# Optimization experiments

Measured on AMD Instinct MI355X. Metric: run time of the kernel, lower is better.

## Reference

```python
import jax, jax.numpy as jnp
import numpy as np

B, C, H, W = 4, 128, 64, 64


def setup_inputs() -> dict:
    key = jax.random.key(0)
    k1, k2 = jax.random.split(key)
    x = jax.random.normal(k1, (B, C, H, W), dtype=jnp.float32)
    # 1x1 conv kv_mapper: weight [C_out, C_in], bias [C_out]; C_out == C_in == C
    W_kv = jax.random.normal(k2, (C, C), dtype=jnp.float32) * (1.0 / np.sqrt(C))
    b_kv = jnp.zeros((C,), dtype=jnp.float32)
    return {"x": x, "W_kv": W_kv, "b_kv": b_kv}


def reference(x, W_kv, b_kv):
    b, c, h, w = x.shape
    # kv_mapper: 1x1 conv  -> v: [b, c, h, w]
    v = jnp.einsum('bchw,oc->bohw', x, W_kv) + b_kv[None, :, None, None]
    # rearrange 'b c h w -> b (h w) c'
    L = h * w
    values = v.reshape(b, c, L).transpose(0, 2, 1)    # keys == values
    queries = x.reshape(b, c, L).transpose(0, 2, 1)
    # scaled dot-product attention, full [b, L, L] scores
    scores = jnp.einsum('blc,btc->blt', queries, values) / jnp.sqrt(jnp.asarray(c, x.dtype))
    attn = jax.nn.softmax(scores, axis=-1)
    out = jnp.einsum('blt,btv->blv', attn, values)    # [b, L, c]
    # rearrange 'b (h w) c -> b c h w'
    return out.transpose(0, 2, 1).reshape(b, c, h, w)
```

## Files before the change

### kernel.cpp

```cpp
#include <hip/hip_runtime.h>

#define LQ 4096
#define CH 128
#define NB 4
#define QSCALE 0.12753139626233174f
#define MAXCH 8
#define TILE_HW 8192

#if defined(__has_builtin)
#if __has_builtin(__builtin_amdgcn_mfma_f32_16x16x16bf16_1k)
#define HAVE_MFMA16 1
#endif
#endif

typedef __attribute__((ext_vector_type(8))) unsigned short ushort8;
typedef __attribute__((ext_vector_type(4))) unsigned short ushort4v;
typedef __attribute__((ext_vector_type(4))) short short4v;
typedef __attribute__((ext_vector_type(8))) __bf16 bf16x8;
typedef __attribute__((ext_vector_type(4))) float f32x4;

__device__ inline unsigned short f2bf(float f) {
    unsigned int u = __builtin_bit_cast(unsigned int, f);
    u += 0x7fffu + ((u >> 16) & 1u);
    return (unsigned short)(u >> 16);
}
__device__ inline float bf2f(unsigned short h) {
    unsigned int u = (unsigned int)h << 16;
    return __builtin_bit_cast(float, u);
}
__device__ inline unsigned int bfpack2(float a, float b) {
    unsigned int ua = __builtin_bit_cast(unsigned int, a) + 0x8000u;
    unsigned int ub = __builtin_bit_cast(unsigned int, b) + 0x8000u;
    return (ua >> 16) | (ub & 0xffff0000u);
}
__device__ inline void gload_lds16(const unsigned short* g, unsigned short* l) {
    __builtin_amdgcn_global_load_lds(
        (const __attribute__((address_space(1))) unsigned int*)(g),
        (__attribute__((address_space(3))) unsigned int*)(l), 16, 0, 0);
}

__global__ __launch_bounds__(256) void prep_kernel(
    const float* __restrict__ x, const float* __restrict__ Wkv,
    const float* __restrict__ bkv,
    unsigned short* __restrict__ Vt2, unsigned short* __restrict__ Vc2)
{
    __shared__ __align__(16) unsigned short xs[64 * 136];
    __shared__ __align__(16) unsigned short vs[128 * 72];
    const int tid = threadIdx.x;
    const int lane = tid & 63;
    const int wave = tid >> 6;
    const int quad = lane >> 4, l16 = lane & 15;
    const int b = blockIdx.x & 3;
    const int T = blockIdx.x >> 2;
    const int l0 = T << 6;

    {
        const f32x4* xg4 = (const f32x4*)(x + (size_t)b * CH * LQ + l0);
        #pragma unroll
        for (int i = 0; i < 8; ++i) {
            int idx = i * 256 + tid;
            int c = idx >> 4, l4 = idx & 15;
            f32x4 v = xg4[c * (LQ / 4) + l4];
            #pragma unroll
            for (int m = 0; m < 4; ++m) xs[(l4 * 4 + m) * 136 + c] = f2bf(v[m]);
        }
    }
    __syncthreads();

    const int wo = wave * 32;
    f32x4 acc[2][4];
    #pragma unroll
    for (int ot = 0; ot < 2; ++ot)
        #pragma unroll
        for (int lt = 0; lt < 4; ++lt) acc[ot][lt] = f32x4{0.f, 0.f, 0.f, 0.f};

    #pragma unroll
    for (int kc = 0; kc < 4; ++kc) {
        bf16x8 af[2];
        #pragma unroll
        for (int ot = 0; ot < 2; ++ot) {
            const float* wrow = Wkv + (size_t)(wo + ot * 16 + l16) * CH + kc * 32 + quad * 8;
            ushort8 a;
            #pragma unroll
            for (int j = 0; j < 8; ++j) a[j] = f2bf(wrow[j]);
            af[ot] = __builtin_bit_cast(bf16x8, a);
        }
        #pragma unroll
        for (int lt = 0; lt < 4; ++lt) {
            bf16x8 bf = __builtin_bit_cast(bf16x8,
                *(const ushort8*)(xs + (lt * 16 + l16) * 136 + kc * 32 + quad * 8));
            #pragma unroll
            for (int ot = 0; ot < 2; ++ot)
                acc[ot][lt] = __builtin_amdgcn_mfma_f32_16x16x32_bf16(af[ot], bf, acc[ot][lt], 0, 0, 0);
        }
    }
    #pragma unroll
    for (int ot = 0; ot < 2; ++ot) {
        float bias[4];
        #pragma unroll
        for (int r = 0; r < 4; ++r) bias[r] = bkv[wo + ot * 16 + quad * 4 + r];
        #pragma unroll
        for (int lt = 0; lt < 4; ++lt)
            #pragma unroll
            for (int r = 0; r < 4; ++r)
                vs[(wo + ot * 16 + quad * 4 + r) * 72 + lt * 16 + l16] =
                    f2bf(acc[ot][lt][r] + bias[r]);
    }
    __syncthreads();
    const size_t tbase = ((size_t)b * 64 + T) * TILE_HW;
    #pragma unroll
    for (int i = 0; i < 4; ++i) {
        const int ci = i * 256 + tid;
        const int g = ci >> 6, ls = ci & 63;
        const int nt = g >> 2, kc = g & 3, qs = ls >> 4, l16s = ls & 15;
        ushort8 v;
        #pragma unroll
        for (int j = 0; j < 8; ++j) v[j] = vs[(kc * 32 + qs * 8 + j) * 72 + nt * 16 + l16s];
        *(ushort8*)(Vt2 + tbase + (size_t)ci * 8) = v;
    }
    #pragma unroll
    for (int i = 0; i < 4; ++i) {
        const int ci = i * 256 + tid;
        const int g = ci >> 6, ls = ci & 63;
        const int nt = g >> 2, p = g & 3, qs = ls >> 4, l16s = ls & 15;
        ushort4v a = *(const ushort4v*)(vs + (p * 32 + l16s) * 72 + nt * 16 + qs * 4);
        ushort4v c2 = *(const ushort4v*)(vs + (p * 32 + 16 + l16s) * 72 + nt * 16 + qs * 4);
        ushort8 v;
        #pragma unroll
        for (int j = 0; j < 4; ++j) { v[j] = a[j]; v[j + 4] = c2[j]; }
        *(ushort8*)(Vc2 + tbase + (size_t)ci * 8) = v;
    }
}

__global__ __launch_bounds__(256) void attn_kernel(
    const float* __restrict__ x, const unsigned short* __restrict__ Vt2,
    const unsigned short* __restrict__ Vc2,
    unsigned short* __restrict__ Opart, float* __restrict__ Lsum, int titers)
{
    __shared__ __align__(16) unsigned short bufA[2][TILE_HW];
    __shared__ __align__(16) unsigned short bufB[2][TILE_HW];
    const int tid = threadIdx.x;
    const int wave = tid >> 6, lane = tid & 63;
    const int quad = lane >> 4, l16 = lane & 15;
    const int b = blockIdx.x & 3;
    const int rest = blockIdx.x >> 2;
    const int qtile = rest & 31;
    const int chunk = rest >> 5;
    const int q0w = (qtile << 7) + (wave << 5);
    const int Tbase = chunk * titers;

    const unsigned short* vtb = Vt2 + (size_t)b * 64 * TILE_HW;
    const unsigned short* vcb = Vc2 + (size_t)b * 64 * TILE_HW;

    bf16x8 qf[2][4];
    #pragma unroll
    for (int mt = 0; mt < 2; ++mt)
        #pragma unroll
        for (int kc = 0; kc < 4; ++kc) {
            ushort8 v;
            #pragma unroll
            for (int j = 0; j < 8; ++j) {
                int c = kc * 32 + quad * 8 + j;
                v[j] = f2bf(x[((size_t)b * CH + c) * LQ + q0w + mt * 16 + l16] * QSCALE);
            }
            qf[mt][kc] = __builtin_bit_cast(bf16x8, v);
        }

    f32x4 oacc[2][8];
    #pragma unroll
    for (int mt = 0; mt < 2; ++mt)
        #pragma unroll
        for (int i = 0; i < 8; ++i) oacc[mt][i] = f32x4{0.f, 0.f, 0.f, 0.f};
    float lsum[2] = {0.f, 0.f};

    auto issue = [&](int T, int nb) {
        const unsigned short* sa = vtb + (size_t)T * TILE_HW + lane * 8;
        const unsigned short* sb = vcb + (size_t)T * TILE_HW + lane * 8;
        #pragma unroll
        for (int g = 0; g < 4; ++g) {
            const int go = (wave * 4 + g) * 512;
            gload_lds16(sa + go, &bufA[nb][go]);
            gload_lds16(sb + go, &bufB[nb][go]);
        }
    };
    issue(Tbase, 0);

    for (int it = 0; it < titers; ++it) {
        __syncthreads();
        if (it + 1 < titers) issue(Tbase + it + 1, (it + 1) & 1);
        const unsigned short* A = bufA[it & 1];
        const unsigned short* B = bufB[it & 1];

        f32x4 s[2][4];
        #pragma unroll
        for (int nt = 0; nt < 4; ++nt) {
            bf16x8 vA[4];
            #pragma unroll
            for (int kc = 0; kc < 4; ++kc)
                vA[kc] = __builtin_bit_cast(bf16x8,
                    *(const ushort8*)(A + (nt * 4 + kc) * 512 + lane * 8));
            #pragma unroll
            for (int mt = 0; mt < 2; ++mt) {
                s[mt][nt] = f32x4{0.f, 0.f, 0.f, 0.f};
                #pragma unroll
                for (int kc = 0; kc < 4; ++kc)
                    s[mt][nt] = __builtin_amdgcn_mfma_f32_16x16x32_bf16(
                        vA[kc], qf[mt][kc], s[mt][nt], 0, 0, 0);
            }
        }
#ifdef HAVE_MFMA16
        short4v pf[2][4];
#else
        bf16x8 pf[2][4];
#endif
        #pragma unroll
        for (int nt = 0; nt < 4; ++nt)
            #pragma unroll
            for (int mt = 0; mt < 2; ++mt) {
                float p0 = __builtin_amdgcn_exp2f(s[mt][nt][0]);
                float p1 = __builtin_amdgcn_exp2f(s[mt][nt][1]);
                float p2 = __builtin_amdgcn_exp2f(s[mt][nt][2]);
                float p3 = __builtin_amdgcn_exp2f(s[mt][nt][3]);
                lsum[mt] += (p0 + p1) + (p2 + p3);
                unsigned int lo = bfpack2(p0, p1);
                unsigned int hi = bfpack2(p2, p3);
#ifdef HAVE_MFMA16
                ushort4v pk;
                pk[0] = (unsigned short)lo; pk[1] = (unsigned short)(lo >> 16);
                pk[2] = (unsigned short)hi; pk[3] = (unsigned short)(hi >> 16);
                pf[mt][nt] = __builtin_bit_cast(short4v, pk);
#else
                ushort8 pk;
                pk[0] = (unsigned short)lo; pk[1] = (unsigned short)(lo >> 16);
                pk[2] = (unsigned short)hi; pk[3] = (unsigned short)(hi >> 16);
                pk[4] = 0; pk[5] = 0; pk[6] = 0; pk[7] = 0;
                pf[mt][nt] = __builtin_bit_cast(bf16x8, pk);
#endif
            }
        #pragma unroll
        for (int nt = 0; nt < 4; ++nt) {
            #pragma unroll
            for (int p = 0; p < 4; ++p) {
                ushort8 d8 = *(const ushort8*)(B + (nt * 4 + p) * 512 + lane * 8);
                #pragma unroll
                for (int h = 0; h < 2; ++h) {
                    ushort4v f;
                    #pragma unroll
                    for (int j = 0; j < 4; ++j) f[j] = d8[h * 4 + j];
#ifdef HAVE_MFMA16
                    short4v vB = __builtin_bit_cast(short4v, f);
                    #pragma unroll
                    for (int mt = 0; mt < 2; ++mt)
                        oacc[mt][p * 2 + h] = __builtin_amdgcn_mfma_f32_16x16x16bf16_1k(
                            pf[mt][nt], vB, oacc[mt][p * 2 + h], 0, 0, 0);
#else
                    ushort8 vb;
                    #pragma unroll
                    for (int j = 0; j < 4; ++j) { vb[j] = f[j]; vb[j + 4] = 0; }
                    bf16x8 vB = __builtin_bit_cast(bf16x8, vb);
                    #pragma unroll
                    for (int mt = 0; mt < 2; ++mt)
                        oacc[mt][p * 2 + h] = __builtin_amdgcn_mfma_f32_16x16x32_bf16(
                            pf[mt][nt], vB, oacc[mt][p * 2 + h], 0, 0, 0);
#endif
                }
            }
        }
    }
    const size_t pbase = ((size_t)(chunk * NB + b) * LQ);
    #pragma unroll
    for (int mt = 0; mt < 2; ++mt) {
        float v = lsum[mt];
        v += __shfl_xor(v, 16);
        v += __shfl_xor(v, 32);
        if (lane < 16) Lsum[pbase + q0w + mt * 16 + lane] = v;
    }
    #pragma unroll
    for (int mt = 0; mt < 2; ++mt)
        #pragma unroll
        for (int r = 0; r < 4; ++r) {
            const int q = q0w + mt * 16 + quad * 4 + r;
            unsigned short* orow = Opart + (pbase + q) * CH + l16;
            #pragma unroll
            for (int nc = 0; nc < 8; ++nc) orow[nc * 16] = f2bf(oacc[mt][nc][r]);
        }
}

__global__ __launch_bounds__(256) void combine_kernel(
    const unsigned short* __restrict__ Opart, const float* __restrict__ Lsum,
    float* __restrict__ out, int nchunk)
{
    __shared__ __align__(16) float ls[32 * 132];
    __shared__ float linv[32];
    const int tid = threadIdx.x;
    const int b = blockIdx.x & 3;
    const int q0 = (blockIdx.x >> 2) << 5;

    if (tid < 32) {
        float s = 0.f;
        for (int ch = 0; ch < nchunk; ++ch) s += Lsum[(size_t)(ch * NB + b) * LQ + q0 + tid];
        linv[tid] = 1.0f / s;
    }
    __syncthreads();
    {
        const int c8 = (tid & 15) * 8, qg = tid >> 4;
        #pragma unroll
        for (int i = 0; i < 2; ++i) {
            const int q = qg * 2 + i;
            float s[8];
            #pragma unroll
            for (int k = 0; k < 8; ++k) s[k] = 0.f;
            for (int ch = 0; ch < nchunk; ++ch) {
                ushort8 p = *(const ushort8*)(Opart +
                    ((size_t)(ch * NB + b) * LQ + q0 + q) * CH + c8);
                #pragma unroll
                for (int k = 0; k < 8; ++k) s[k] += bf2f(p[k]);
            }
            const float li = linv[q];
            f32x4 o0, o1;
            #pragma unroll
            for (int k = 0; k < 4; ++k) { o0[k] = s[k] * li; o1[k] = s[k + 4] * li; }
            *(f32x4*)(ls + q * 132 + c8) = o0;
            *(f32x4*)(ls + q * 132 + c8 + 4) = o1;
        }
    }
    __syncthreads();
    {
        const int c = tid & 127, qh = tid >> 7;
        float* dst = out + ((size_t)b * CH + c) * LQ + q0 + qh * 16;
        #pragma unroll
        for (int i = 0; i < 4; ++i) {
            f32x4 o;
            #pragma unroll
            for (int r = 0; r < 4; ++r) o[r] = ls[(qh * 16 + i * 4 + r) * 132 + c];
            ((f32x4*)dst)[i] = o;
        }
    }
}

extern "C" void kernel_launch(void* const* d_in, const int* in_sizes, int n_in,
                              void* d_out, int out_size, void* d_ws, size_t ws_size,
                              hipStream_t stream) {
    const float* x   = (const float*)d_in[0];
    const float* Wkv = (const float*)d_in[1];
    const float* bkv = (const float*)d_in[2];
    float* out = (float*)d_out;

    const size_t vElems = (size_t)NB * LQ * CH;
    unsigned short* Vt2 = (unsigned short*)d_ws;
    unsigned short* Vc2 = Vt2 + vElems;
    float* Lsum = (float*)(Vc2 + vElems);
    unsigned short* Opart = (unsigned short*)(Lsum + (size_t)MAXCH * NB * LQ);

    int nchunk = 4;
    const size_t fixed = 2 * vElems * 2 + (size_t)MAXCH * NB * LQ * 4;
    while (nchunk > 1 && fixed + (size_t)nchunk * NB * LQ * CH * 2 > ws_size) nchunk >>= 1;
    const int titers = (LQ / 64) / nchunk;

    prep_kernel<<<dim3(256), dim3(256), 0, stream>>>(x, Wkv, bkv, Vt2, Vc2);
    attn_kernel<<<dim3(128 * nchunk), dim3(256), 0, stream>>>(x, Vt2, Vc2, Opart, Lsum, titers);
    combine_kernel<<<dim3(512), dim3(256), 0, stream>>>(Opart, Lsum, out, nchunk);
}
```

Before: 122.1 us.

## Single-buffer A tile, add mid-iteration sync, raise occupancy and chunk count

The A (key) tile becomes single-buffered and its next load is issued after a second barrier that follows the QK^T phase. This cuts LDS use from 64KB to 48KB per block so three blocks can fit per CU, which the new launch bound requests. The probability fragments are now built per nt inside the PV loop, which lowers register pressure. The number of key chunks goes from 4 to 8, doubling the grid. The cost is an extra barrier per iteration, less time to hide the A-tile load, and more partial outputs for the combine kernel to merge.

```diff
diff --git a/kernel.cpp b/kernel.cpp
--- a/kernel.cpp
+++ b/kernel.cpp
@@ -132,12 +132,12 @@
     }
 }
 
-__global__ __launch_bounds__(256) void attn_kernel(
+__global__ __launch_bounds__(256, 3) void attn_kernel(
     const float* __restrict__ x, const unsigned short* __restrict__ Vt2,
     const unsigned short* __restrict__ Vc2,
     unsigned short* __restrict__ Opart, float* __restrict__ Lsum, int titers)
 {
-    __shared__ __align__(16) unsigned short bufA[2][TILE_HW];
+    __shared__ __align__(16) unsigned short bufA[TILE_HW];
     __shared__ __align__(16) unsigned short bufB[2][TILE_HW];
     const int tid = threadIdx.x;
     const int wave = tid >> 6, lane = tid & 63;
@@ -173,22 +173,28 @@
         for (int i = 0; i < 8; ++i) oacc[mt][i] = f32x4{0.f, 0.f, 0.f, 0.f};
     float lsum[2] = {0.f, 0.f};
 
-    auto issue = [&](int T, int nb) {
+    auto issueA = [&](int T) {
         const unsigned short* sa = vtb + (size_t)T * TILE_HW + lane * 8;
-        const unsigned short* sb = vcb + (size_t)T * TILE_HW + lane * 8;
         #pragma unroll
         for (int g = 0; g < 4; ++g) {
             const int go = (wave * 4 + g) * 512;
-            gload_lds16(sa + go, &bufA[nb][go]);
+            gload_lds16(sa + go, &bufA[go]);
+        }
+    };
+    auto issueB = [&](int T, int nb) {
+        const unsigned short* sb = vcb + (size_t)T * TILE_HW + lane * 8;
+        #pragma unroll
+        for (int g = 0; g < 4; ++g) {
+            const int go = (wave * 4 + g) * 512;
             gload_lds16(sb + go, &bufB[nb][go]);
         }
     };
-    issue(Tbase, 0);
+    issueA(Tbase);
+    issueB(Tbase, 0);
 
     for (int it = 0; it < titers; ++it) {
         __syncthreads();
-        if (it + 1 < titers) issue(Tbase + it + 1, (it + 1) & 1);
-        const unsigned short* A = bufA[it & 1];
+        if (it + 1 < titers) issueB(it + 1 + Tbase, (it + 1) & 1);
         const unsigned short* B = bufB[it & 1];
 
         f32x4 s[2][4];
@@ -198,7 +204,7 @@
             #pragma unroll
             for (int kc = 0; kc < 4; ++kc)
                 vA[kc] = __builtin_bit_cast(bf16x8,
-                    *(const ushort8*)(A + (nt * 4 + kc) * 512 + lane * 8));
+                    *(const ushort8*)(bufA + (nt * 4 + kc) * 512 + lane * 8));
             #pragma unroll
             for (int mt = 0; mt < 2; ++mt) {
                 s[mt][nt] = f32x4{0.f, 0.f, 0.f, 0.f};
@@ -208,13 +214,16 @@
                         vA[kc], qf[mt][kc], s[mt][nt], 0, 0, 0);
             }
         }
+        __syncthreads();
+        if (it + 1 < titers) issueA(it + 1 + Tbase);
+
+        #pragma unroll
+        for (int nt = 0; nt < 4; ++nt) {
 #ifdef HAVE_MFMA16
-        short4v pf[2][4];
+            short4v pf[2];
 #else
-        bf16x8 pf[2][4];
-#endif
-        #pragma unroll
-        for (int nt = 0; nt < 4; ++nt)
+            bf16x8 pf[2];
+#endif
             #pragma unroll
             for (int mt = 0; mt < 2; ++mt) {
                 float p0 = __builtin_amdgcn_exp2f(s[mt][nt][0]);
@@ -228,17 +237,15 @@
                 ushort4v pk;
                 pk[0] = (unsigned short)lo; pk[1] = (unsigned short)(lo >> 16);
                 pk[2] = (unsigned short)hi; pk[3] = (unsigned short)(hi >> 16);
-                pf[mt][nt] = __builtin_bit_cast(short4v, pk);
+                pf[mt] = __builtin_bit_cast(short4v, pk);
 #else
                 ushort8 pk;
                 pk[0] = (unsigned short)lo; pk[1] = (unsigned short)(lo >> 16);
                 pk[2] = (unsigned short)hi; pk[3] = (unsigned short)(hi >> 16);
                 pk[4] = 0; pk[5] = 0; pk[6] = 0; pk[7] = 0;
-                pf[mt][nt] = __builtin_bit_cast(bf16x8, pk);
-#endif
-            }
-        #pragma unroll
-        for (int nt = 0; nt < 4; ++nt) {
+                pf[mt] = __builtin_bit_cast(bf16x8, pk);
+#endif
+            }
             #pragma unroll
             for (int p = 0; p < 4; ++p) {
                 ushort8 d8 = *(const ushort8*)(B + (nt * 4 + p) * 512 + lane * 8);
@@ -252,7 +259,7 @@
                     #pragma unroll
                     for (int mt = 0; mt < 2; ++mt)
                         oacc[mt][p * 2 + h] = __builtin_amdgcn_mfma_f32_16x16x16bf16_1k(
-                            pf[mt][nt], vB, oacc[mt][p * 2 + h], 0, 0, 0);
+                            pf[mt], vB, oacc[mt][p * 2 + h], 0, 0, 0);
 #else
                     ushort8 vb;
                     #pragma unroll
@@ -261,7 +268,7 @@
                     #pragma unroll
                     for (int mt = 0; mt < 2; ++mt)
                         oacc[mt][p * 2 + h] = __builtin_amdgcn_mfma_f32_16x16x32_bf16(
-                            pf[mt][nt], vB, oacc[mt][p * 2 + h], 0, 0, 0);
+                            pf[mt], vB, oacc[mt][p * 2 + h], 0, 0, 0);
 #endif
                 }
             }
@@ -352,7 +359,7 @@
     float* Lsum = (float*)(Vc2 + vElems);
     unsigned short* Opart = (unsigned short*)(Lsum + (size_t)MAXCH * NB * LQ);
 
-    int nchunk = 4;
+    int nchunk = MAXCH;
     const size_t fixed = 2 * vElems * 2 + (size_t)MAXCH * NB * LQ * 4;
     while (nchunk > 1 && fixed + (size_t)nchunk * NB * LQ * CH * 2 > ws_size) nchunk >>= 1;
     const int titers = (LQ / 64) / nchunk;
```

After: 125.2 us. 1.03x slower.
